# Kernel tuning notes

Hardware: AMD Instinct MI355X
Metric: run time of the kernel (lower is better)

## Reference

```python
import jax, jax.numpy as jnp
import numpy as np

N_NODES = 100000


def _graph_conv(x, W, b, src, dst, n_nodes):
    # DGL GraphConv, norm='both', weight applied before aggregation (in>out).
    E = src.shape[0]
    ones = jnp.ones((E,), dtype=x.dtype)
    out_deg = jax.ops.segment_sum(ones, src, num_segments=n_nodes)
    in_deg = jax.ops.segment_sum(ones, dst, num_segments=n_nodes)
    out_norm = jnp.clip(out_deg, 1.0, None) ** -0.5  # [N]
    in_norm = jnp.clip(in_deg, 1.0, None) ** -0.5    # [N]
    h = (x * out_norm[:, None]) @ W                  # [N, out] dense GEMM first
    msg = h[src]                                     # gather  [E, out]
    agg = jax.ops.segment_sum(msg, dst, num_segments=n_nodes)  # scatter-add
    return agg * in_norm[:, None] + b


def setup_inputs() -> dict:
    key = jax.random.key(0)
    k1, k2, k3, k4, k5 = jax.random.split(key, 5)
    E = 1600000
    features = jax.random.normal(k1, (N_NODES, 128), dtype=jnp.float32)
    src = jax.random.randint(k2, (E,), 0, N_NODES, dtype=jnp.int64)
    dst = jax.random.randint(k3, (E,), 0, N_NODES, dtype=jnp.int64)
    W1 = jax.random.normal(k4, (128, 64), dtype=jnp.float32) * (1.0 / np.sqrt(128))
    b1 = jnp.zeros((64,), dtype=jnp.float32)
    W2 = jax.random.normal(k5, (64, 32), dtype=jnp.float32) * (1.0 / np.sqrt(64))
    b2 = jnp.zeros((32,), dtype=jnp.float32)
    return {"features": features, "src": src, "dst": dst,
            "W1": W1, "b1": b1, "W2": W2, "b2": b2}


def reference(features, src, dst, W1, b1, W2, b2):
    x = jax.nn.relu(_graph_conv(features, W1, b1, src, dst, N_NODES))
    x = _graph_conv(x, W2, b2, src, dst, N_NODES)
    return x
```

## Files before the change

### kernel.cpp

```cpp
#include <hip/hip_runtime.h>
#include <hip/hip_bf16.h>


#define BSH 7
#define BNODES 128
#define SRCMASK 0x1FFFF
#define CAP 2560
#define CHUNK 4096

typedef __attribute__((ext_vector_type(8))) short bf16x8;
typedef __attribute__((ext_vector_type(4))) float f32x4;

__device__ __forceinline__ unsigned short f2bf(float f) {
    unsigned int u = __float_as_uint(f);
    return (unsigned short)((u + 0x7FFFu + ((u >> 16) & 1u)) >> 16);
}

__device__ __forceinline__ float bflo(unsigned int u) {
    return __uint_as_float(u << 16);
}
__device__ __forceinline__ float bfhi(unsigned int u) {
    return __uint_as_float(u & 0xFFFF0000u);
}

__global__ __launch_bounds__(1024) void k_place(const int* __restrict__ src,
        const int* __restrict__ dst, int* __restrict__ ebuf,
        unsigned char* __restrict__ sbuf, int* __restrict__ offs,
        int* __restrict__ soffs, int E) {
    __shared__ int lh[800], s[800];
    int t = threadIdx.x;
    int e0 = blockIdx.x * CHUNK;
    int nE = min(CHUNK, E - e0);
    int sv[4], dv[4];
#pragma unroll
    for (int j = 0; j < 4; j++) {
        int i = t + 1024 * j;
        if (i < nE) { sv[j] = src[e0 + i]; dv[j] = dst[e0 + i]; }
        else        { sv[j] = -1; }
    }
    if (t < 800) lh[t] = 0;
    __syncthreads();
#pragma unroll
    for (int j = 0; j < 4; j++) if (sv[j] >= 0) {
        atomicAdd(&lh[dv[j] >> BSH], 0x10000);
        atomicAdd(&lh[sv[j] >> BSH], 1);
    }
    __syncthreads();
    if (t < 800) s[t] = lh[t];
    __syncthreads();
    for (int o = 1; o < 800; o <<= 1) {
        int u = (t < 800 && t >= o) ? s[t - o] : 0;
        __syncthreads();
        if (t < 800) s[t] += u;
        __syncthreads();
    }
    int obase = blockIdx.x * 801;
    if (t < 800) {
        int incl = s[t], c = lh[t];
        int bd = (incl >> 16) - (c >> 16);
        int bs = (incl & 0xFFFF) - (c & 0xFFFF);
        offs[obase + t] = bd;
        soffs[obase + t] = bs;
        s[t] = (bd << 16) | bs;
    }
    if (t == 0) { offs[obase + 800] = nE; soffs[obase + 800] = nE; }
    __syncthreads();
#pragma unroll
    for (int j = 0; j < 4; j++) if (sv[j] >= 0) {
        int pd = atomicAdd(&s[dv[j] >> BSH], 0x10000) >> 16;
        ebuf[e0 + pd] = sv[j] | ((dv[j] & (BNODES - 1)) << 17);
        int ps = atomicAdd(&s[sv[j] >> BSH], 1) & 0xFFFF;
        sbuf[e0 + ps] = (unsigned char)(sv[j] & (BNODES - 1));
    }
}

__global__ __launch_bounds__(1024) void k_sort2(const int* __restrict__ ebuf,
        const unsigned char* __restrict__ sbuf, const int* __restrict__ offs,
        const int* __restrict__ soffs, int* __restrict__ csrc,
        int* __restrict__ ostart, int* __restrict__ oend,
        float* __restrict__ nI, float* __restrict__ nO, int n, int NBLK) {
    __shared__ int cnt2[264], scnt2[264], cur2[264];
    __shared__ int cnt[BNODES], s[BNODES];
    __shared__ int segst[400], segen[400], sst[400], sen[400];
    int t = threadIdx.x, b = blockIdx.x;
    if (t < NBLK) {
        segst[t] = t * CHUNK + offs[t * 801 + b];
        segen[t] = t * CHUNK + offs[t * 801 + b + 1];
        sst[t]   = t * CHUNK + soffs[t * 801 + b];
        sen[t]   = t * CHUNK + soffs[t * 801 + b + 1];
    }
    if (t < 264) { cnt2[t] = 0; scnt2[t] = 0; }
    __syncthreads();
    int grp = t >> 3, ln = t & 7;
    int hb = (t >> 9) * 132;
    for (int sg = grp; sg < NBLK; sg += 128) {
        int en = segen[sg];
        for (int i = segst[sg] + ln; i < en; i += 8)
            atomicAdd(&cnt2[hb + (ebuf[i] >> 17)], 1);
        int en2 = sen[sg];
        for (int i = sst[sg] + ln; i < en2; i += 8)
            atomicAdd(&scnt2[hb + sbuf[i]], 1);
    }
    __syncthreads();
    if (t < BNODES) {
        cnt[t] = cnt2[t] + cnt2[132 + t];
        s[t] = cnt[t];
    }
    __syncthreads();
    for (int o = 1; o < BNODES; o <<= 1) {
        int u = (t < BNODES && t >= o) ? s[t - o] : 0;
        __syncthreads();
        if (t < BNODES) s[t] += u;
        __syncthreads();
    }
    if (t < BNODES) {
        int e0 = b * CAP;
        int st = e0 + s[t] - cnt[t];
        cur2[t] = st;
        cur2[132 + t] = st + cnt2[t];
        int g = b * BNODES + t;
        if (g < n) {
            ostart[g] = st;
            oend[g] = e0 + s[t];
            nI[g] = rsqrtf(fmaxf((float)cnt[t], 1.0f));
            int sct = scnt2[t] + scnt2[132 + t];
            nO[g] = rsqrtf(fmaxf((float)sct, 1.0f));
        }
    }
    __syncthreads();
    for (int sg = grp; sg < NBLK; sg += 128) {
        int en = segen[sg];
        for (int i = segst[sg] + ln; i < en; i += 8) {
            int p = ebuf[i];
            int pos = atomicAdd(&cur2[hb + (p >> 17)], 1);
            csrc[pos] = p & SRCMASK;
        }
    }
}

__global__ __launch_bounds__(256) void k_gemm1(const float* __restrict__ x,
                        const float* __restrict__ W1, const float* __restrict__ nO,
                        unsigned short* __restrict__ h1, int n) {
    __shared__ __align__(16) unsigned short sX[64 * 136];
    __shared__ __align__(16) unsigned short sWT[64 * 136];
    const int t = threadIdx.x;
    {
        const float4* W4 = (const float4*)W1;
#pragma unroll
        for (int i = 0; i < 8; i++) {
            int f = t + 256 * i;
            int k = f >> 4, n4 = (f & 15) * 4;
            float4 v = W4[f];
            sWT[(n4 + 0) * 136 + k] = f2bf(v.x);
            sWT[(n4 + 1) * 136 + k] = f2bf(v.y);
            sWT[(n4 + 2) * 136 + k] = f2bf(v.z);
            sWT[(n4 + 3) * 136 + k] = f2bf(v.w);
        }
    }
    const int rowbase = blockIdx.x * 64;
    {
        const float4* x4 = (const float4*)x;
#pragma unroll
        for (int i = 0; i < 8; i++) {
            int f = t + 256 * i;
            int row = f >> 5, kc = f & 31;
            int grow = rowbase + row;
            float4 v = make_float4(0.f, 0.f, 0.f, 0.f);
            float sc = 0.f;
            if (grow < n) { v = x4[(size_t)grow * 32 + kc]; sc = nO[grow]; }
            ushort4 o;
            o.x = f2bf(v.x * sc); o.y = f2bf(v.y * sc);
            o.z = f2bf(v.z * sc); o.w = f2bf(v.w * sc);
            *(ushort4*)&sX[row * 136 + kc * 4] = o;
        }
    }
    __syncthreads();
    const int wv = t >> 6, lane = t & 63;
    const int lr = lane & 15, lk = lane >> 4;
    const int m0 = wv * 16;
    f32x4 acc0 = {0.f, 0.f, 0.f, 0.f};
    f32x4 acc1 = {0.f, 0.f, 0.f, 0.f};
    f32x4 acc2 = {0.f, 0.f, 0.f, 0.f};
    f32x4 acc3 = {0.f, 0.f, 0.f, 0.f};
#pragma unroll
    for (int kk = 0; kk < 4; kk++) {
        bf16x8 a = *(const bf16x8*)&sX[(m0 + lr) * 136 + kk * 32 + lk * 8];
        bf16x8 b0 = *(const bf16x8*)&sWT[(0 * 16 + lr) * 136 + kk * 32 + lk * 8];
        bf16x8 b1 = *(const bf16x8*)&sWT[(1 * 16 + lr) * 136 + kk * 32 + lk * 8];
        bf16x8 b2 = *(const bf16x8*)&sWT[(2 * 16 + lr) * 136 + kk * 32 + lk * 8];
        bf16x8 b3 = *(const bf16x8*)&sWT[(3 * 16 + lr) * 136 + kk * 32 + lk * 8];
        acc0 = __builtin_amdgcn_mfma_f32_16x16x32_bf16(a, b0, acc0, 0, 0, 0);
        acc1 = __builtin_amdgcn_mfma_f32_16x16x32_bf16(a, b1, acc1, 0, 0, 0);
        acc2 = __builtin_amdgcn_mfma_f32_16x16x32_bf16(a, b2, acc2, 0, 0, 0);
        acc3 = __builtin_amdgcn_mfma_f32_16x16x32_bf16(a, b3, acc3, 0, 0, 0);
    }
#pragma unroll
    for (int i = 0; i < 4; i++) {
        int grow = rowbase + m0 + lk * 4 + i;
        if (grow < n) {
            size_t base = (size_t)grow * 64 + lr;
            h1[base]      = f2bf(acc0[i]);
            h1[base + 16] = f2bf(acc1[i]);
            h1[base + 32] = f2bf(acc2[i]);
            h1[base + 48] = f2bf(acc3[i]);
        }
    }
}

__global__ void k_agg64(const unsigned short* __restrict__ h,
                        const int* __restrict__ csrc,
                        const int* __restrict__ ostart, const int* __restrict__ oend,
                        const float* __restrict__ nI, const float* __restrict__ b1,
                        float* __restrict__ x2, int n) {
    int node = blockIdx.x * 4 + (threadIdx.x >> 6);
    int lane = threadIdx.x & 63;
    if (node >= n) return;
    int s0 = ostart[node], s1 = oend[node];
    int sub = lane >> 3;
    int c8 = (lane & 7) * 8;
    float a[8] = {}, d[8] = {};
    int e = s0;
    for (; e + 15 < s1; e += 16) {
        int p0 = csrc[e + sub];
        int p1 = csrc[e + 8 + sub];
        uint4 u0 = *(const uint4*)&h[(size_t)p0 * 64 + c8];
        uint4 u1 = *(const uint4*)&h[(size_t)p1 * 64 + c8];
        a[0] += bflo(u0.x); a[1] += bfhi(u0.x);
        a[2] += bflo(u0.y); a[3] += bfhi(u0.y);
        a[4] += bflo(u0.z); a[5] += bfhi(u0.z);
        a[6] += bflo(u0.w); a[7] += bfhi(u0.w);
        d[0] += bflo(u1.x); d[1] += bfhi(u1.x);
        d[2] += bflo(u1.y); d[3] += bfhi(u1.y);
        d[4] += bflo(u1.z); d[5] += bfhi(u1.z);
        d[6] += bflo(u1.w); d[7] += bfhi(u1.w);
    }
    for (; e < s1; e += 8) {
        if (e + sub < s1) {
            int p = csrc[e + sub];
            uint4 u = *(const uint4*)&h[(size_t)p * 64 + c8];
            a[0] += bflo(u.x); a[1] += bfhi(u.x);
            a[2] += bflo(u.y); a[3] += bfhi(u.y);
            a[4] += bflo(u.z); a[5] += bfhi(u.z);
            a[6] += bflo(u.w); a[7] += bfhi(u.w);
        }
    }
#pragma unroll
    for (int i = 0; i < 8; i++) a[i] += d[i];
#pragma unroll
    for (int i = 0; i < 8; i++) {
        a[i] += __shfl(a[i], lane ^ 8, 64);
        a[i] += __shfl(a[i], lane ^ 16, 64);
        a[i] += __shfl(a[i], lane ^ 32, 64);
    }
    if (sub == 0) {
        float ni = nI[node];
        float4 o0, o1;
        o0.x = fmaxf(fmaf(a[0], ni, b1[c8 + 0]), 0.f);
        o0.y = fmaxf(fmaf(a[1], ni, b1[c8 + 1]), 0.f);
        o0.z = fmaxf(fmaf(a[2], ni, b1[c8 + 2]), 0.f);
        o0.w = fmaxf(fmaf(a[3], ni, b1[c8 + 3]), 0.f);
        o1.x = fmaxf(fmaf(a[4], ni, b1[c8 + 4]), 0.f);
        o1.y = fmaxf(fmaf(a[5], ni, b1[c8 + 5]), 0.f);
        o1.z = fmaxf(fmaf(a[6], ni, b1[c8 + 6]), 0.f);
        o1.w = fmaxf(fmaf(a[7], ni, b1[c8 + 7]), 0.f);
        *(float4*)&x2[(size_t)node * 64 + c8] = o0;
        *(float4*)&x2[(size_t)node * 64 + c8 + 4] = o1;
    }
}

__global__ __launch_bounds__(256) void k_gemm2(const float* __restrict__ x2,
                        const float* __restrict__ W2, const float* __restrict__ nO,
                        unsigned short* __restrict__ h2, int n) {
    __shared__ float sX[128 * 68];
    __shared__ float sW[64 * 32];
    const int t = threadIdx.x;
    {
        const float4* W4 = (const float4*)W2;
        float4* sW4 = (float4*)sW;
#pragma unroll
        for (int i = 0; i < 2; i++) sW4[t + 256 * i] = W4[t + 256 * i];
    }
    const int rowbase = blockIdx.x * 128;
    {
        const float4* x4 = (const float4*)x2;
        float4* sX4 = (float4*)sX;
#pragma unroll
        for (int i = 0; i < 8; i++) {
            int f = t + 256 * i;
            int row = f >> 4, kc = f & 15;
            int grow = rowbase + row;
            float4 v = make_float4(0.f, 0.f, 0.f, 0.f);
            if (grow < n) v = x4[(size_t)grow * 16 + kc];
            sX4[row * 17 + kc] = v;
        }
    }
    __syncthreads();
    const int lane = t & 63, wv = t >> 6;
    const int whalf = wv >> 1, chalf = wv & 1;
    const int rg = lane >> 2, cg = lane & 3;
    const int c0 = chalf * 16 + cg * 4;
    const int rloc = whalf * 64 + rg;
    float acc[4][4] = {};
    for (int kk = 0; kk < 64; kk += 4) {
        float xr[4][4], wr[4][4];
#pragma unroll
        for (int i = 0; i < 4; i++)
            *(float4*)xr[i] = *(const float4*)&sX[(rloc + 16 * i) * 68 + kk];
#pragma unroll
        for (int j = 0; j < 4; j++)
            *(float4*)wr[j] = *(const float4*)&sW[(kk + j) * 32 + c0];
#pragma unroll
        for (int j = 0; j < 4; j++)
#pragma unroll
            for (int i = 0; i < 4; i++)
#pragma unroll
                for (int c = 0; c < 4; c++)
                    acc[i][c] = fmaf(xr[i][j], wr[j][c], acc[i][c]);
    }
#pragma unroll
    for (int i = 0; i < 4; i++) {
        int grow = rowbase + rloc + 16 * i;
        if (grow < n) {
            float nf = nO[grow];
            ushort4 o;
            o.x = f2bf(acc[i][0] * nf); o.y = f2bf(acc[i][1] * nf);
            o.z = f2bf(acc[i][2] * nf); o.w = f2bf(acc[i][3] * nf);
            *(ushort4*)&h2[(size_t)grow * 32 + c0] = o;
        }
    }
}

__global__ void k_agg32(const unsigned short* __restrict__ h,
                        const int* __restrict__ csrc,
                        const int* __restrict__ ostart, const int* __restrict__ oend,
                        const float* __restrict__ nI, const float* __restrict__ b2,
                        float* __restrict__ out, int n) {
    int node = blockIdx.x * 4 + (threadIdx.x >> 6);
    int lane = threadIdx.x & 63;
    if (node >= n) return;
    int s0 = ostart[node], s1 = oend[node];
    int sub = lane >> 2;
    int c8 = (lane & 3) * 8;
    float a[8] = {};
    int e = s0;
    for (; e + 15 < s1; e += 16) {
        int p = csrc[e + sub];
        uint4 u = *(const uint4*)&h[(size_t)p * 32 + c8];
        a[0] += bflo(u.x); a[1] += bfhi(u.x);
        a[2] += bflo(u.y); a[3] += bfhi(u.y);
        a[4] += bflo(u.z); a[5] += bfhi(u.z);
        a[6] += bflo(u.w); a[7] += bfhi(u.w);
    }
    for (; e < s1; e += 16) {
        if (e + sub < s1) {
            int p = csrc[e + sub];
            uint4 u = *(const uint4*)&h[(size_t)p * 32 + c8];
            a[0] += bflo(u.x); a[1] += bfhi(u.x);
            a[2] += bflo(u.y); a[3] += bfhi(u.y);
            a[4] += bflo(u.z); a[5] += bfhi(u.z);
            a[6] += bflo(u.w); a[7] += bfhi(u.w);
        }
    }
#pragma unroll
    for (int i = 0; i < 8; i++) {
        a[i] += __shfl(a[i], lane ^ 4, 64);
        a[i] += __shfl(a[i], lane ^ 8, 64);
        a[i] += __shfl(a[i], lane ^ 16, 64);
        a[i] += __shfl(a[i], lane ^ 32, 64);
    }
    if (sub == 0) {
        float ni = nI[node];
        float4 o0, o1;
        o0.x = fmaf(a[0], ni, b2[c8 + 0]);
        o0.y = fmaf(a[1], ni, b2[c8 + 1]);
        o0.z = fmaf(a[2], ni, b2[c8 + 2]);
        o0.w = fmaf(a[3], ni, b2[c8 + 3]);
        o1.x = fmaf(a[4], ni, b2[c8 + 4]);
        o1.y = fmaf(a[5], ni, b2[c8 + 5]);
        o1.z = fmaf(a[6], ni, b2[c8 + 6]);
        o1.w = fmaf(a[7], ni, b2[c8 + 7]);
        *(float4*)&out[(size_t)node * 32 + c8] = o0;
        *(float4*)&out[(size_t)node * 32 + c8 + 4] = o1;
    }
}

extern "C" void kernel_launch(void* const* d_in, const int* in_sizes, int n_in,
                              void* d_out, int out_size, void* d_ws, size_t ws_size,
                              hipStream_t stream) {
    const float* x   = (const float*)d_in[0];
    const int*   src = (const int*)d_in[1];
    const int*   dst = (const int*)d_in[2];
    const float* W1  = (const float*)d_in[3];
    const float* b1  = (const float*)d_in[4];
    const float* W2  = (const float*)d_in[5];
    const float* b2  = (const float*)d_in[6];
    float* out = (float*)d_out;

    const int N = in_sizes[0] / 128;
    const int E = in_sizes[1];
    const int NB = (N + BNODES - 1) / BNODES;
    const int NBLK = (E + CHUNK - 1) / CHUNK;

    char* wsb = (char*)d_ws;
    float* nO     = (float*)wsb;  wsb += (size_t)N * 4;
    float* nI     = (float*)wsb;  wsb += (size_t)N * 4;
    int*   ostart = (int*)wsb;    wsb += (size_t)N * 4;
    int*   oend   = (int*)wsb;    wsb += (size_t)N * 4;
    int*   csrc   = (int*)wsb;    wsb += (size_t)NB * CAP * 4;
    int*   offs   = (int*)wsb;    wsb += (size_t)NBLK * 801 * 4;
    unsigned short* h1 = (unsigned short*)wsb;
                                  wsb += (size_t)N * 64 * 2;
    float* x2     = (float*)wsb;  wsb += (size_t)N * 64 * 4;
    unsigned short* h2 = h1;
    int*   ebuf   = (int*)x2;
    unsigned char* sbuf = (unsigned char*)(ebuf) + (size_t)E * 4;
    int*   soffs  = (int*)(sbuf + (size_t)E);

    k_place<<<NBLK, 1024, 0, stream>>>(src, dst, ebuf, sbuf, offs, soffs, E);
    k_sort2<<<NB, 1024, 0, stream>>>(ebuf, sbuf, offs, soffs, csrc,
                                     ostart, oend, nI, nO, N, NBLK);

    k_gemm1<<<(N + 63) / 64, 256, 0, stream>>>(x, W1, nO, h1, N);
    k_agg64<<<(N + 3) / 4, 256, 0, stream>>>(h1, csrc, ostart, oend, nI, b1, x2, N);

    k_gemm2<<<(N + 127) / 128, 256, 0, stream>>>(x2, W2, nO, h2, N);
    k_agg32<<<(N + 3) / 4, 256, 0, stream>>>(h2, csrc, ostart, oend, nI, b2, out, N);
}
```

Baseline: 277.4 us.

## Fuse first GEMM into sort kernel and move second GEMM to bf16 MFMA

The layer-1 dense GEMM now runs inside the per-bucket sort kernel. Each 128-node bucket block computes its out-degree norms, keeps them in shared memory and applies them directly to its rows of x, which removes one kernel launch and a global round-trip of nO. The second GEMM switches from an FP32 FMA tile loop to bf16 MFMA, with the out-norm scaling applied on input instead of output. The trade-offs are more shared memory per sort block, which may cut occupancy, and lower precision in the second GEMM.

```diff
diff --git a/kernel.cpp b/kernel.cpp
--- a/kernel.cpp
+++ b/kernel.cpp
@@ -74,15 +74,21 @@
     }
 }
 
-__global__ __launch_bounds__(1024) void k_sort2(const int* __restrict__ ebuf,
+__global__ __launch_bounds__(1024) void k_sg1(const int* __restrict__ ebuf,
         const unsigned char* __restrict__ sbuf, const int* __restrict__ offs,
         const int* __restrict__ soffs, int* __restrict__ csrc,
         int* __restrict__ ostart, int* __restrict__ oend,
-        float* __restrict__ nI, float* __restrict__ nO, int n, int NBLK) {
+        float* __restrict__ nI, float* __restrict__ nO,
+        const float* __restrict__ x, const float* __restrict__ W1,
+        unsigned short* __restrict__ h1, int n, int NBLK) {
     __shared__ int cnt2[264], scnt2[264], cur2[264];
     __shared__ int cnt[BNODES], s[BNODES];
     __shared__ int segst[400], segen[400], sst[400], sen[400];
+    __shared__ float snO[BNODES];
+    __shared__ __align__(16) unsigned short sX[128 * 136];
+    __shared__ __align__(16) unsigned short sWT[64 * 136];
     int t = threadIdx.x, b = blockIdx.x;
+
     if (t < NBLK) {
         segst[t] = t * CHUNK + offs[t * 801 + b];
         segen[t] = t * CHUNK + offs[t * 801 + b + 1];
@@ -118,13 +124,15 @@
         int st = e0 + s[t] - cnt[t];
         cur2[t] = st;
         cur2[132 + t] = st + cnt2[t];
+        int sct = scnt2[t] + scnt2[132 + t];
+        float nov = rsqrtf(fmaxf((float)sct, 1.0f));
+        snO[t] = nov;
         int g = b * BNODES + t;
         if (g < n) {
             ostart[g] = st;
             oend[g] = e0 + s[t];
             nI[g] = rsqrtf(fmaxf((float)cnt[t], 1.0f));
-            int sct = scnt2[t] + scnt2[132 + t];
-            nO[g] = rsqrtf(fmaxf((float)sct, 1.0f));
+            nO[g] = nov;
         }
     }
     __syncthreads();
@@ -136,19 +144,13 @@
             csrc[pos] = p & SRCMASK;
         }
     }
-}
-
-__global__ __launch_bounds__(256) void k_gemm1(const float* __restrict__ x,
-                        const float* __restrict__ W1, const float* __restrict__ nO,
-                        unsigned short* __restrict__ h1, int n) {
-    __shared__ __align__(16) unsigned short sX[64 * 136];
-    __shared__ __align__(16) unsigned short sWT[64 * 136];
-    const int t = threadIdx.x;
+
+    __syncthreads();
     {
         const float4* W4 = (const float4*)W1;
 #pragma unroll
-        for (int i = 0; i < 8; i++) {
-            int f = t + 256 * i;
+        for (int i = 0; i < 2; i++) {
+            int f = t + 1024 * i;
             int k = f >> 4, n4 = (f & 15) * 4;
             float4 v = W4[f];
             sWT[(n4 + 0) * 136 + k] = f2bf(v.x);
@@ -157,17 +159,17 @@
             sWT[(n4 + 3) * 136 + k] = f2bf(v.w);
         }
     }
-    const int rowbase = blockIdx.x * 64;
+    const int rowbase = b * BNODES;
     {
         const float4* x4 = (const float4*)x;
 #pragma unroll
-        for (int i = 0; i < 8; i++) {
-            int f = t + 256 * i;
+        for (int i = 0; i < 4; i++) {
+            int f = t + 1024 * i;
             int row = f >> 5, kc = f & 31;
             int grow = rowbase + row;
             float4 v = make_float4(0.f, 0.f, 0.f, 0.f);
             float sc = 0.f;
-            if (grow < n) { v = x4[(size_t)grow * 32 + kc]; sc = nO[grow]; }
+            if (grow < n) { v = x4[(size_t)grow * 32 + kc]; sc = snO[row]; }
             ushort4 o;
             o.x = f2bf(v.x * sc); o.y = f2bf(v.y * sc);
             o.z = f2bf(v.z * sc); o.w = f2bf(v.w * sc);
@@ -177,32 +179,25 @@
     __syncthreads();
     const int wv = t >> 6, lane = t & 63;
     const int lr = lane & 15, lk = lane >> 4;
-    const int m0 = wv * 16;
+    const int slab = (wv & 7) * 16;
+    const int ch = (wv >> 3) * 32;
     f32x4 acc0 = {0.f, 0.f, 0.f, 0.f};
     f32x4 acc1 = {0.f, 0.f, 0.f, 0.f};
-    f32x4 acc2 = {0.f, 0.f, 0.f, 0.f};
-    f32x4 acc3 = {0.f, 0.f, 0.f, 0.f};
 #pragma unroll
     for (int kk = 0; kk < 4; kk++) {
-        bf16x8 a = *(const bf16x8*)&sX[(m0 + lr) * 136 + kk * 32 + lk * 8];
-        bf16x8 b0 = *(const bf16x8*)&sWT[(0 * 16 + lr) * 136 + kk * 32 + lk * 8];
-        bf16x8 b1 = *(const bf16x8*)&sWT[(1 * 16 + lr) * 136 + kk * 32 + lk * 8];
-        bf16x8 b2 = *(const bf16x8*)&sWT[(2 * 16 + lr) * 136 + kk * 32 + lk * 8];
-        bf16x8 b3 = *(const bf16x8*)&sWT[(3 * 16 + lr) * 136 + kk * 32 + lk * 8];
+        bf16x8 a  = *(const bf16x8*)&sX[(slab + lr) * 136 + kk * 32 + lk * 8];
+        bf16x8 b0 = *(const bf16x8*)&sWT[(ch + lr) * 136 + kk * 32 + lk * 8];
+        bf16x8 b1 = *(const bf16x8*)&sWT[(ch + 16 + lr) * 136 + kk * 32 + lk * 8];
         acc0 = __builtin_amdgcn_mfma_f32_16x16x32_bf16(a, b0, acc0, 0, 0, 0);
         acc1 = __builtin_amdgcn_mfma_f32_16x16x32_bf16(a, b1, acc1, 0, 0, 0);
-        acc2 = __builtin_amdgcn_mfma_f32_16x16x32_bf16(a, b2, acc2, 0, 0, 0);
-        acc3 = __builtin_amdgcn_mfma_f32_16x16x32_bf16(a, b3, acc3, 0, 0, 0);
     }
 #pragma unroll
     for (int i = 0; i < 4; i++) {
-        int grow = rowbase + m0 + lk * 4 + i;
+        int grow = rowbase + slab + lk * 4 + i;
         if (grow < n) {
-            size_t base = (size_t)grow * 64 + lr;
+            size_t base = (size_t)grow * 64 + ch + lr;
             h1[base]      = f2bf(acc0[i]);
             h1[base + 16] = f2bf(acc1[i]);
-            h1[base + 32] = f2bf(acc2[i]);
-            h1[base + 48] = f2bf(acc3[i]);
         }
     }
 }
@@ -271,61 +266,69 @@
 __global__ __launch_bounds__(256) void k_gemm2(const float* __restrict__ x2,
                         const float* __restrict__ W2, const float* __restrict__ nO,
                         unsigned short* __restrict__ h2, int n) {
-    __shared__ float sX[128 * 68];
-    __shared__ float sW[64 * 32];
+    __shared__ __align__(16) unsigned short sX[128 * 72];
+    __shared__ __align__(16) unsigned short sWT[32 * 72];
     const int t = threadIdx.x;
     {
         const float4* W4 = (const float4*)W2;
-        float4* sW4 = (float4*)sW;
-#pragma unroll
-        for (int i = 0; i < 2; i++) sW4[t + 256 * i] = W4[t + 256 * i];
+#pragma unroll
+        for (int i = 0; i < 2; i++) {
+            int f = t + 256 * i;
+            int k = f >> 3, n4 = (f & 7) * 4;
+            float4 v = W4[f];
+            sWT[(n4 + 0) * 72 + k] = f2bf(v.x);
+            sWT[(n4 + 1) * 72 + k] = f2bf(v.y);
+            sWT[(n4 + 2) * 72 + k] = f2bf(v.z);
+            sWT[(n4 + 3) * 72 + k] = f2bf(v.w);
+        }
     }
     const int rowbase = blockIdx.x * 128;
     {
         const float4* x4 = (const float4*)x2;
-        float4* sX4 = (float4*)sX;
 #pragma unroll
         for (int i = 0; i < 8; i++) {
             int f = t + 256 * i;
             int row = f >> 4, kc = f & 15;
             int grow = rowbase + row;
             float4 v = make_float4(0.f, 0.f, 0.f, 0.f);
-            if (grow < n) v = x4[(size_t)grow * 16 + kc];
-            sX4[row * 17 + kc] = v;
-        }
-    }
-    __syncthreads();
-    const int lane = t & 63, wv = t >> 6;
-    const int whalf = wv >> 1, chalf = wv & 1;
-    const int rg = lane >> 2, cg = lane & 3;
-    const int c0 = chalf * 16 + cg * 4;
-    const int rloc = whalf * 64 + rg;
-    float acc[4][4] = {};
-    for (int kk = 0; kk < 64; kk += 4) {
-        float xr[4][4], wr[4][4];
-#pragma unroll
-        for (int i = 0; i < 4; i++)
-            *(float4*)xr[i] = *(const float4*)&sX[(rloc + 16 * i) * 68 + kk];
-#pragma unroll
-        for (int j = 0; j < 4; j++)
-            *(float4*)wr[j] = *(const float4*)&sW[(kk + j) * 32 + c0];
-#pragma unroll
-        for (int j = 0; j < 4; j++)
-#pragma unroll
-            for (int i = 0; i < 4; i++)
-#pragma unroll
-                for (int c = 0; c < 4; c++)
-                    acc[i][c] = fmaf(xr[i][j], wr[j][c], acc[i][c]);
+            float sc = 0.f;
+            if (grow < n) { v = x4[(size_t)grow * 16 + kc]; sc = nO[grow]; }
+            ushort4 o;
+            o.x = f2bf(v.x * sc); o.y = f2bf(v.y * sc);
+            o.z = f2bf(v.z * sc); o.w = f2bf(v.w * sc);
+            *(ushort4*)&sX[row * 72 + kc * 4] = o;
+        }
+    }
+    __syncthreads();
+    const int wv = t >> 6, lane = t & 63;
+    const int lr = lane & 15, lk = lane >> 4;
+    const int slab = wv * 32;
+    f32x4 a00 = {0.f, 0.f, 0.f, 0.f};
+    f32x4 a01 = {0.f, 0.f, 0.f, 0.f};
+    f32x4 a10 = {0.f, 0.f, 0.f, 0.f};
+    f32x4 a11 = {0.f, 0.f, 0.f, 0.f};
+#pragma unroll
+    for (int kk = 0; kk < 2; kk++) {
+        bf16x8 a0 = *(const bf16x8*)&sX[(slab + lr) * 72 + kk * 32 + lk * 8];
+        bf16x8 a1 = *(const bf16x8*)&sX[(slab + 16 + lr) * 72 + kk * 32 + lk * 8];
+        bf16x8 b0 = *(const bf16x8*)&sWT[lr * 72 + kk * 32 + lk * 8];
+        bf16x8 b1 = *(const bf16x8*)&sWT[(16 + lr) * 72 + kk * 32 + lk * 8];
+        a00 = __builtin_amdgcn_mfma_f32_16x16x32_bf16(a0, b0, a00, 0, 0, 0);
+        a01 = __builtin_amdgcn_mfma_f32_16x16x32_bf16(a0, b1, a01, 0, 0, 0);
+        a10 = __builtin_amdgcn_mfma_f32_16x16x32_bf16(a1, b0, a10, 0, 0, 0);
+        a11 = __builtin_amdgcn_mfma_f32_16x16x32_bf16(a1, b1, a11, 0, 0, 0);
     }
 #pragma unroll
     for (int i = 0; i < 4; i++) {
-        int grow = rowbase + rloc + 16 * i;
-        if (grow < n) {
-            float nf = nO[grow];
-            ushort4 o;
-            o.x = f2bf(acc[i][0] * nf); o.y = f2bf(acc[i][1] * nf);
-            o.z = f2bf(acc[i][2] * nf); o.w = f2bf(acc[i][3] * nf);
-            *(ushort4*)&h2[(size_t)grow * 32 + c0] = o;
+        int g0 = rowbase + slab + lk * 4 + i;
+        if (g0 < n) {
+            h2[(size_t)g0 * 32 + lr]      = f2bf(a00[i]);
+            h2[(size_t)g0 * 32 + 16 + lr] = f2bf(a01[i]);
+        }
+        int g1 = g0 + 16;
+        if (g1 < n) {
+            h2[(size_t)g1 * 32 + lr]      = f2bf(a10[i]);
+            h2[(size_t)g1 * 32 + 16 + lr] = f2bf(a11[i]);
         }
     }
 }
@@ -417,10 +420,9 @@
     int*   soffs  = (int*)(sbuf + (size_t)E);
 
     k_place<<<NBLK, 1024, 0, stream>>>(src, dst, ebuf, sbuf, offs, soffs, E);
-    k_sort2<<<NB, 1024, 0, stream>>>(ebuf, sbuf, offs, soffs, csrc,
-                                     ostart, oend, nI, nO, N, NBLK);
-
-    k_gemm1<<<(N + 63) / 64, 256, 0, stream>>>(x, W1, nO, h1, N);
+    k_sg1<<<NB, 1024, 0, stream>>>(ebuf, sbuf, offs, soffs, csrc,
+                                   ostart, oend, nI, nO, x, W1, h1, N, NBLK);
+
     k_agg64<<<(N + 3) / 4, 256, 0, stream>>>(h1, csrc, ostart, oend, nI, b1, x2, N);
 
     k_gemm2<<<(N + 127) / 128, 256, 0, stream>>>(x2, W2, nO, h2, N);
```

New measurement: 249.4 us. -10.1%, faster.
